# Kernel tuning notes

Measured on AMD Instinct MI355X. Metric: run time of the kernel, lower is better.

Reference implementation:

```python
import jax, jax.numpy as jnp
import numpy as np

# Render constants matching GaussianRenderer(__init__): image size and top-K blend depth.
H, W, K = 128, 128, 10
N_G = 2048  # number of gaussians


def setup_inputs() -> dict:
    key = jax.random.key(0)
    k1, k2, k3, k4 = jax.random.split(key, 4)
    # Means in pixel coordinates so gaussians cover the image.
    gaussian_means = jax.random.uniform(k1, (N_G, 2), dtype=jnp.float32) * jnp.array([W, H], jnp.float32)
    # Rotation angle per gaussian in [0, 2pi).
    gaussian_rotations = jax.random.uniform(k2, (N_G,), dtype=jnp.float32) * (2.0 * np.pi)
    # log std-devs centered at log(3) => ~3px footprint.
    gaussian_log_scales = jax.random.normal(k3, (N_G, 2), dtype=jnp.float32) * 0.3 + np.log(3.0)
    gaussian_colors = jax.random.uniform(k4, (N_G, 3), dtype=jnp.float32)
    return {
        "gaussian_means": gaussian_means,
        "gaussian_rotations": gaussian_rotations,
        "gaussian_log_scales": gaussian_log_scales,
        "gaussian_colors": gaussian_colors,
    }


def reference(gaussian_means, gaussian_rotations, gaussian_log_scales, gaussian_colors):
    """2D Gaussian splatting: per-pixel top-K gaussians by opacity, alpha-composited.

    Covariance per gaussian: Sigma = R(theta) diag(exp(2*log_scales)) R(theta)^T.
    alpha_i(p) = exp(-0.5 * d^T Sigma^{-1} d), d = p - mean_i.
    Per pixel, the K gaussians with largest alpha are blended front-to-back:
        out = sum_i color_i * alpha_i * prod_{j<i} (1 - alpha_j).
    (The torch module's tile binning + max_G_per_tile is a GPU performance
    optimization; the dense evaluation here computes the same per-pixel math.)
    """
    cos_t = jnp.cos(gaussian_rotations)  # [N]
    sin_t = jnp.sin(gaussian_rotations)
    inv_var = jnp.exp(-2.0 * gaussian_log_scales)  # [N,2] = 1/sigma^2 per axis
    ivx, ivy = inv_var[:, 0], inv_var[:, 1]
    # Sigma^{-1} = R diag(1/sx^2, 1/sy^2) R^T  (symmetric 2x2: [[a, b], [b, c]])
    a = cos_t * cos_t * ivx + sin_t * sin_t * ivy  # [N]
    c = sin_t * sin_t * ivx + cos_t * cos_t * ivy
    b = cos_t * sin_t * (ivx - ivy)

    xs = jnp.arange(W, dtype=jnp.float32) + 0.5
    ys = jnp.arange(H, dtype=jnp.float32) + 0.5
    px, py = jnp.meshgrid(xs, ys)  # [H,W] each
    dx = px.reshape(-1, 1) - gaussian_means[:, 0]  # [P, N], P = H*W
    dy = py.reshape(-1, 1) - gaussian_means[:, 1]
    q = a * dx * dx + 2.0 * b * dx * dy + c * dy * dy  # Mahalanobis distance^2 [P,N]
    alpha = jnp.exp(-0.5 * q)  # [P,N] in (0,1]

    top_alpha, top_idx = jax.lax.top_k(alpha, K)  # [P,K], descending alpha
    # Front-to-back transmittance: T_0 = 1, T_i = prod_{j<i} (1 - alpha_j)
    trans = jnp.cumprod(1.0 - top_alpha, axis=1)
    trans = jnp.concatenate([jnp.ones_like(trans[:, :1]), trans[:, :-1]], axis=1)
    weight = top_alpha * trans  # [P,K]
    top_colors = gaussian_colors[top_idx]  # [P,K,3]
    image = jnp.einsum("pk,pkc->pc", weight, top_colors).reshape(H, W, 3)
    return image
```

## Files before the change

kernel.cpp:

```cpp
#include <hip/hip_runtime.h>

#define HH 128
#define WW 128
#define NPX (HH * WW)
#define KK 10
#define PXB 16
#define LCAP 352
#define JMAX 22
#define KEYC 6
#define SCAP (16 * KEYC)
#define SPAD (SCAP + 1)
#define ALPHA_MIN 5e-4f
#define RADIUS_K 3.8990f

typedef unsigned long long u64;
typedef unsigned int u32;

__device__ __forceinline__ u64 umax64(u64 a, u64 b) { return a > b ? a : b; }

template <int NGC>
__global__ __launch_bounds__(256) void splat_kernel(
    const float* __restrict__ means, const float* __restrict__ rots,
    const float* __restrict__ lscales, const float* __restrict__ cols,
    int nG_rt, float* __restrict__ out) {
  const int nG = NGC > 0 ? NGC : nG_rt;
  __shared__ float4 sA[LCAP];
  __shared__ float  sMy[LCAP];
  __shared__ int    glist[LCAP];
  __shared__ float2 sbuf[PXB][SPAD];
  __shared__ int    lcnt;

  int t = threadIdx.x;
  int lane = t & 63;
  int pl  = t >> 4;
  int tsl = t & 15;
  int tile = blockIdx.x;
  int x0 = (tile & 31) << 2, y0 = (tile >> 5) << 2;
  int x = x0 | (pl & 3), y = y0 | (pl >> 2);
  float px = (float)x + 0.5f, py = (float)y + 0.5f;

  if (t == 0) lcnt = 0;
  __syncthreads();

  const float2* m2 = (const float2*)means;
  const float2* l2 = (const float2*)lscales;
  float rx0 = (float)x0 + 0.5f, rx1 = (float)x0 + 3.5f;
  float ry0 = (float)y0 + 0.5f, ry1 = (float)y0 + 3.5f;
  for (int g = t; g < nG; g += 256) {
    float2 mg = m2[g];
    float2 lg = l2[g];
    float smx = __expf(fmaxf(lg.x, lg.y));
    float r = fmaf(RADIUS_K * 1.01f, smx, 0.05f);
    float cx = fminf(fmaxf(mg.x, rx0), rx1) - mg.x;
    float cy = fminf(fmaxf(mg.y, ry0), ry1) - mg.y;
    bool hit = (cx * cx + cy * cy <= r * r);
    u64 mask = __ballot(hit);
    if (mask) {
      int leader = __ffsll((unsigned long long)mask) - 1;
      int base;
      if (lane == leader) base = atomicAdd(&lcnt, __popcll(mask));
      base = __shfl(base, leader);
      if (hit) {
        int idx = base + __popcll(mask & ((1ull << lane) - 1ull));
        if (idx < LCAP) {
          float th = rots[g];
          float s = __sinf(th), c = __cosf(th);
          float ivx = __expf(-2.0f * lg.x);
          float ivy = __expf(-2.0f * lg.y);
          sA[idx] = make_float4(c * c * ivx + s * s * ivy,
                                2.0f * (c * s * (ivx - ivy)),
                                s * s * ivx + c * c * ivy, mg.x);
          sMy[idx] = mg.y;
          glist[idx] = g;
        }
      }
    }
  }
  __syncthreads();
  int cnt = min(lcnt, LCAP);

  float ra[JMAX];
  float mymax = 0.0f;
#pragma unroll
  for (int j = 0; j < JMAX; ++j) {
    int i = tsl + j * 16;
    float a = 0.0f;
    if (i < cnt) {
      float4 q0 = sA[i];
      float dx = px - q0.w, dy = py - sMy[i];
      float q = fmaf(dx, fmaf(q0.y, dy, q0.x * dx), q0.z * dy * dy);
      a = __expf(-0.5f * q);
    }
    ra[j] = a;
    mymax = fmaxf(mymax, a);
  }

  float tv[KK];
#pragma unroll
  for (int k = 0; k < KK; ++k) tv[k] = 0.0f;
#pragma unroll
  for (int i = 0; i < 16; ++i) {
    float v = __shfl(mymax, i, 16);
#pragma unroll
    for (int k = 0; k < KK; ++k) {
      float tvk = tv[k];
      bool sw = v > tvk;
      tv[k] = sw ? v : tvk;
      v = sw ? tvk : v;
    }
  }
  float tau = fmaxf(tv[KK - 1], ALPHA_MIN);

  int cpx = 0;
  int grp = lane >> 4;
#pragma unroll
  for (int j = 0; j < JMAX; ++j) {
    bool s = ra[j] >= tau;
    u64 mask = __ballot(s);
    u32 sub = (u32)((mask >> (grp * 16)) & 0xFFFFull);
    if (s) {
      int idx = cpx + __popc(sub & ((1u << tsl) - 1u));
      if (idx < SCAP)
        sbuf[pl][idx] = make_float2(ra[j], __int_as_float(glist[tsl + j * 16]));
    }
    cpx += __popc(sub);
  }
  int scp = min(cpx, SCAP);

  u64 keys[KEYC];
#pragma unroll
  for (int c = 0; c < KEYC; ++c) {
    int i = tsl + c * 16;
    u64 kk = 0;
    if (i < scp) {
      float2 e = sbuf[pl][i];
      kk = ((u64)__float_as_uint(e.x) << 32) | (u32)(~(u32)__float_as_int(e.y));
    }
    keys[c] = kk;
  }

  float my_alpha = 0.0f;
  int my_id = 0;
#pragma unroll
  for (int r = 0; r < KK; ++r) {
    u64 m = keys[0];
#pragma unroll
    for (int c = 1; c < KEYC; ++c) m = umax64(m, keys[c]);
#pragma unroll
    for (int d = 1; d < 16; d <<= 1)
      m = umax64(m, (u64)__shfl_xor((unsigned long long)m, d));
#pragma unroll
    for (int c = 0; c < KEYC; ++c)
      if (keys[c] == m) keys[c] = 0;
    if (tsl == r && m != 0) {
      my_alpha = __uint_as_float((u32)(m >> 32));
      my_id = (int)(~(u32)m);
    }
  }

  float T = 1.0f - my_alpha;
#pragma unroll
  for (int d = 1; d < 16; d <<= 1) {
    float u = __shfl_up(T, d, 16);
    if (tsl >= d) T *= u;
  }
  float ex = __shfl_up(T, 1, 16);
  if (tsl == 0) ex = 1.0f;
  float w = my_alpha * ex;
  float cr = 0.0f, cg = 0.0f, cb = 0.0f;
  if (my_alpha > 0.0f) {
    cr = w * cols[3 * my_id + 0];
    cg = w * cols[3 * my_id + 1];
    cb = w * cols[3 * my_id + 2];
  }
#pragma unroll
  for (int d = 1; d < 16; d <<= 1) {
    cr += __shfl_xor(cr, d);
    cg += __shfl_xor(cg, d);
    cb += __shfl_xor(cb, d);
  }
  int p = y * WW + x;
  if (tsl < 3) out[3 * p + tsl] = (tsl == 0) ? cr : ((tsl == 1) ? cg : cb);
}

extern "C" void kernel_launch(void* const* d_in, const int* in_sizes, int n_in,
                              void* d_out, int out_size, void* d_ws, size_t ws_size,
                              hipStream_t stream) {
  const float* means   = (const float*)d_in[0];
  const float* rots    = (const float*)d_in[1];
  const float* lscales = (const float*)d_in[2];
  const float* cols    = (const float*)d_in[3];
  float* out = (float*)d_out;
  int nG = in_sizes[1];

  if (nG == 2048) {
    splat_kernel<2048><<<NPX / PXB, 256, 0, stream>>>(means, rots, lscales,
                                                      cols, nG, out);
  } else {
    splat_kernel<0><<<NPX / PXB, 256, 0, stream>>>(means, rots, lscales,
                                                   cols, nG, out);
  }
}
```

Measured before the change: 74.21 us.

## Precompute gaussian params in separate kernel, bitonic threshold, rank-based top-K selection

Adds a precompute kernel that computes each gaussian's squared radius and inverse-covariance coefficients once into workspace, so the 1024 tile blocks no longer redo the exp/sin/cos work per gaussian. It also replaces the insertion-sort tenth-max threshold with a 16-lane bitonic sort and skips empty candidate chunks based on the list count. The iterative 10-round max-extraction is replaced by an O(n^2) rank count through shared memory. The costs are an extra kernel launch, a dependence on workspace being available, and possibly more shared-memory traffic in the rank loop when candidate counts are large.

```diff
diff --git a/kernel.cpp b/kernel.cpp
--- a/kernel.cpp
+++ b/kernel.cpp
@@ -16,18 +16,40 @@
 typedef unsigned long long u64;
 typedef unsigned int u32;
 
-__device__ __forceinline__ u64 umax64(u64 a, u64 b) { return a > b ? a : b; }
-
-template <int NGC>
+__global__ __launch_bounds__(256) void precompute_kernel(
+    const float* __restrict__ means, const float* __restrict__ rots,
+    const float* __restrict__ lscales, int nG,
+    float4* __restrict__ bbox4, float4* __restrict__ prm4) {
+  int g = blockIdx.x * blockDim.x + threadIdx.x;
+  if (g >= nG) return;
+  const float2* m2 = (const float2*)means;
+  const float2* l2 = (const float2*)lscales;
+  float2 mg = m2[g];
+  float2 lg = l2[g];
+  float smx = __expf(fmaxf(lg.x, lg.y));
+  float r = fmaf(RADIUS_K * 1.01f, smx, 0.05f);
+  float th = rots[g];
+  float s = __sinf(th), c = __cosf(th);
+  float ivx = __expf(-2.0f * lg.x);
+  float ivy = __expf(-2.0f * lg.y);
+  bbox4[g] = make_float4(mg.x, mg.y, r * r, mg.y);
+  prm4[g] = make_float4(c * c * ivx + s * s * ivy,
+                        2.0f * (c * s * (ivx - ivy)),
+                        s * s * ivx + c * c * ivy, mg.x);
+}
+
+template <int NGC, bool PRE>
 __global__ __launch_bounds__(256) void splat_kernel(
     const float* __restrict__ means, const float* __restrict__ rots,
     const float* __restrict__ lscales, const float* __restrict__ cols,
+    const float4* __restrict__ bbox4, const float4* __restrict__ prm4,
     int nG_rt, float* __restrict__ out) {
   const int nG = NGC > 0 ? NGC : nG_rt;
   __shared__ float4 sA[LCAP];
   __shared__ float  sMy[LCAP];
   __shared__ int    glist[LCAP];
   __shared__ float2 sbuf[PXB][SPAD];
+  __shared__ float2 wbuf[PXB][KK];
   __shared__ int    lcnt;
 
   int t = threadIdx.x;
@@ -47,13 +69,23 @@
   float rx0 = (float)x0 + 0.5f, rx1 = (float)x0 + 3.5f;
   float ry0 = (float)y0 + 0.5f, ry1 = (float)y0 + 3.5f;
   for (int g = t; g < nG; g += 256) {
-    float2 mg = m2[g];
-    float2 lg = l2[g];
-    float smx = __expf(fmaxf(lg.x, lg.y));
-    float r = fmaf(RADIUS_K * 1.01f, smx, 0.05f);
-    float cx = fminf(fmaxf(mg.x, rx0), rx1) - mg.x;
-    float cy = fminf(fmaxf(mg.y, ry0), ry1) - mg.y;
-    bool hit = (cx * cx + cy * cy <= r * r);
+    bool hit;
+    float4 bb;
+    float2 mg, lg;
+    if (PRE) {
+      bb = bbox4[g];
+      float cx = fminf(fmaxf(bb.x, rx0), rx1) - bb.x;
+      float cy = fminf(fmaxf(bb.y, ry0), ry1) - bb.y;
+      hit = (cx * cx + cy * cy <= bb.z);
+    } else {
+      mg = m2[g];
+      lg = l2[g];
+      float smx = __expf(fmaxf(lg.x, lg.y));
+      float r = fmaf(RADIUS_K * 1.01f, smx, 0.05f);
+      float cx = fminf(fmaxf(mg.x, rx0), rx1) - mg.x;
+      float cy = fminf(fmaxf(mg.y, ry0), ry1) - mg.y;
+      hit = (cx * cx + cy * cy <= r * r);
+    }
     u64 mask = __ballot(hit);
     if (mask) {
       int leader = __ffsll((unsigned long long)mask) - 1;
@@ -63,14 +95,19 @@
       if (hit) {
         int idx = base + __popcll(mask & ((1ull << lane) - 1ull));
         if (idx < LCAP) {
-          float th = rots[g];
-          float s = __sinf(th), c = __cosf(th);
-          float ivx = __expf(-2.0f * lg.x);
-          float ivy = __expf(-2.0f * lg.y);
-          sA[idx] = make_float4(c * c * ivx + s * s * ivy,
-                                2.0f * (c * s * (ivx - ivy)),
-                                s * s * ivx + c * c * ivy, mg.x);
-          sMy[idx] = mg.y;
+          if (PRE) {
+            sA[idx] = prm4[g];
+            sMy[idx] = bb.w;
+          } else {
+            float th = rots[g];
+            float s = __sinf(th), c = __cosf(th);
+            float ivx = __expf(-2.0f * lg.x);
+            float ivy = __expf(-2.0f * lg.y);
+            sA[idx] = make_float4(c * c * ivx + s * s * ivy,
+                                  2.0f * (c * s * (ivx - ivy)),
+                                  s * s * ivx + c * c * ivy, mg.x);
+            sMy[idx] = mg.y;
+          }
           glist[idx] = g;
         }
       }
@@ -78,84 +115,85 @@
   }
   __syncthreads();
   int cnt = min(lcnt, LCAP);
+  int jcnt = (cnt + 15) >> 4;
 
   float ra[JMAX];
   float mymax = 0.0f;
 #pragma unroll
   for (int j = 0; j < JMAX; ++j) {
-    int i = tsl + j * 16;
     float a = 0.0f;
-    if (i < cnt) {
-      float4 q0 = sA[i];
-      float dx = px - q0.w, dy = py - sMy[i];
-      float q = fmaf(dx, fmaf(q0.y, dy, q0.x * dx), q0.z * dy * dy);
-      a = __expf(-0.5f * q);
+    if (j < jcnt) {
+      int i = tsl + (j << 4);
+      if (i < cnt) {
+        float4 q0 = sA[i];
+        float dx = px - q0.w, dy = py - sMy[i];
+        float q = fmaf(dx, fmaf(q0.y, dy, q0.x * dx), q0.z * dy * dy);
+        a = __expf(-0.5f * q);
+      }
     }
     ra[j] = a;
     mymax = fmaxf(mymax, a);
   }
 
-  float tv[KK];
-#pragma unroll
-  for (int k = 0; k < KK; ++k) tv[k] = 0.0f;
-#pragma unroll
-  for (int i = 0; i < 16; ++i) {
-    float v = __shfl(mymax, i, 16);
-#pragma unroll
-    for (int k = 0; k < KK; ++k) {
-      float tvk = tv[k];
-      bool sw = v > tvk;
-      tv[k] = sw ? v : tvk;
-      v = sw ? tvk : v;
-    }
-  }
-  float tau = fmaxf(tv[KK - 1], ALPHA_MIN);
+  float v = mymax;
+#pragma unroll
+  for (int k = 2; k <= 16; k <<= 1) {
+#pragma unroll
+    for (int j = k >> 1; j >= 1; j >>= 1) {
+      float o = __shfl_xor(v, j, 16);
+      bool keepMax = (((tsl & k) == 0) == ((tsl & j) == 0));
+      v = keepMax ? fmaxf(v, o) : fminf(v, o);
+    }
+  }
+  float tau = fmaxf(__shfl(v, 9, 16), ALPHA_MIN);
 
   int cpx = 0;
   int grp = lane >> 4;
 #pragma unroll
   for (int j = 0; j < JMAX; ++j) {
-    bool s = ra[j] >= tau;
-    u64 mask = __ballot(s);
-    u32 sub = (u32)((mask >> (grp * 16)) & 0xFFFFull);
-    if (s) {
-      int idx = cpx + __popc(sub & ((1u << tsl) - 1u));
-      if (idx < SCAP)
-        sbuf[pl][idx] = make_float2(ra[j], __int_as_float(glist[tsl + j * 16]));
-    }
-    cpx += __popc(sub);
+    if (j < jcnt) {
+      bool s = ra[j] >= tau;
+      u64 mask = __ballot(s);
+      u32 sub = (u32)((mask >> (grp * 16)) & 0xFFFFull);
+      if (s) {
+        int idx = cpx + __popc(sub & ((1u << tsl) - 1u));
+        if (idx < SCAP)
+          sbuf[pl][idx] = make_float2(ra[j], __int_as_float(glist[tsl + (j << 4)]));
+      }
+      cpx += __popc(sub);
+    }
   }
   int scp = min(cpx, SCAP);
-
-  u64 keys[KEYC];
+  int nw = min(scp, KK);
+
 #pragma unroll
   for (int c = 0; c < KEYC; ++c) {
-    int i = tsl + c * 16;
-    u64 kk = 0;
-    if (i < scp) {
-      float2 e = sbuf[pl][i];
-      kk = ((u64)__float_as_uint(e.x) << 32) | (u32)(~(u32)__float_as_int(e.y));
-    }
-    keys[c] = kk;
+    if ((c << 4) < scp) {
+      int i = tsl + (c << 4);
+      u64 kc = 0;
+      if (i < scp) {
+        float2 e = sbuf[pl][i];
+        kc = ((u64)__float_as_uint(e.x) << 32) | (u32)(~(u32)__float_as_int(e.y));
+      }
+      int rk = 0;
+      for (int s2 = 0; s2 < scp; ++s2) {
+        float2 e2 = sbuf[pl][s2];
+        u64 ks2 = ((u64)__float_as_uint(e2.x) << 32) |
+                  (u32)(~(u32)__float_as_int(e2.y));
+        rk += (kc < ks2) ? 1 : 0;
+      }
+      if (kc != 0 && rk < KK)
+        wbuf[pl][rk] = make_float2(__uint_as_float((u32)(kc >> 32)),
+                                   __int_as_float((int)(~(u32)kc)));
+    }
   }
 
   float my_alpha = 0.0f;
   int my_id = 0;
-#pragma unroll
-  for (int r = 0; r < KK; ++r) {
-    u64 m = keys[0];
-#pragma unroll
-    for (int c = 1; c < KEYC; ++c) m = umax64(m, keys[c]);
-#pragma unroll
-    for (int d = 1; d < 16; d <<= 1)
-      m = umax64(m, (u64)__shfl_xor((unsigned long long)m, d));
-#pragma unroll
-    for (int c = 0; c < KEYC; ++c)
-      if (keys[c] == m) keys[c] = 0;
-    if (tsl == r && m != 0) {
-      my_alpha = __uint_as_float((u32)(m >> 32));
-      my_id = (int)(~(u32)m);
-    }
+  if (tsl < nw) {
+    float2 e = wbuf[pl][tsl];
+    my_alpha = e.x;
+    my_id = __float_as_int(e.y);
   }
 
   float T = 1.0f - my_alpha;
@@ -193,11 +231,29 @@
   float* out = (float*)d_out;
   int nG = in_sizes[1];
 
+  size_t need = (size_t)nG * sizeof(float4) * 2;
+  bool pre = (d_ws != nullptr) && (ws_size >= need);
+  float4* bbox4 = (float4*)d_ws;
+  float4* prm4 = (float4*)((char*)d_ws + (size_t)nG * sizeof(float4));
+
+  if (pre)
+    precompute_kernel<<<(nG + 255) / 256, 256, 0, stream>>>(means, rots,
+                                                            lscales, nG,
+                                                            bbox4, prm4);
+
   if (nG == 2048) {
-    splat_kernel<2048><<<NPX / PXB, 256, 0, stream>>>(means, rots, lscales,
-                                                      cols, nG, out);
+    if (pre)
+      splat_kernel<2048, true><<<NPX / PXB, 256, 0, stream>>>(
+          means, rots, lscales, cols, bbox4, prm4, nG, out);
+    else
+      splat_kernel<2048, false><<<NPX / PXB, 256, 0, stream>>>(
+          means, rots, lscales, cols, nullptr, nullptr, nG, out);
   } else {
-    splat_kernel<0><<<NPX / PXB, 256, 0, stream>>>(means, rots, lscales,
-                                                   cols, nG, out);
+    if (pre)
+      splat_kernel<0, true><<<NPX / PXB, 256, 0, stream>>>(
+          means, rots, lscales, cols, bbox4, prm4, nG, out);
+    else
+      splat_kernel<0, false><<<NPX / PXB, 256, 0, stream>>>(
+          means, rots, lscales, cols, nullptr, nullptr, nG, out);
   }
 }
```

Result: faster. 70.21 us (-5.4%).
